# Kernel tuning notes

Measured on AMD Instinct MI355X. Metric: run time of the kernel, lower is better.

The kernel has to match this reference:

```python
import jax, jax.numpy as jnp
import numpy as np
from jax.scipy.linalg import expm

B, S, D, E, K, NROT = 2, 2048, 1024, 8, 2, 3
EPS = 1e-5


def setup_inputs() -> dict:
    key = jax.random.key(0)
    ks = jax.random.split(key, 16)
    sc = 0.02
    x = jax.random.normal(ks[0], (B, S, D), jnp.float32)
    ln_gamma = 1.0 + sc * jax.random.normal(ks[1], (D,), jnp.float32)
    ln_beta = sc * jax.random.normal(ks[2], (D,), jnp.float32)
    abel_w = sc * jax.random.normal(ks[3], (D, D), jnp.float32)
    abel_b = sc * jax.random.normal(ks[4], (D,), jnp.float32)
    moe_gate_w = sc * jax.random.normal(ks[5], (D, E), jnp.float32)
    moe_gate_b = sc * jax.random.normal(ks[6], (E,), jnp.float32)
    ew1 = sc * jax.random.normal(ks[7], (E, D, 2 * D), jnp.float32)
    eb1 = sc * jax.random.normal(ks[8], (E, 2 * D), jnp.float32)
    ew2 = sc * jax.random.normal(ks[9], (E, 2 * D, D), jnp.float32)
    eb2 = sc * jax.random.normal(ks[10], (E, D), jnp.float32)
    g = sc * jax.random.normal(ks[11], (NROT, D, D), jnp.float32)
    gens = 0.5 * (g - jnp.swapaxes(g, -1, -2))  # skew-symmetric, as in reset_parameters
    gc_w = sc * jax.random.normal(ks[12], (2 * D, 1), jnp.float32)
    gc_b = sc * jax.random.normal(ks[13], (1,), jnp.float32)
    return dict(x=x, ln_gamma=ln_gamma, ln_beta=ln_beta, abel_w=abel_w, abel_b=abel_b,
                moe_gate_w=moe_gate_w, moe_gate_b=moe_gate_b, ew1=ew1, eb1=eb1,
                ew2=ew2, eb2=eb2, gens=gens, gc_w=gc_w, gc_b=gc_b)


def _gelu(x):
    return jax.nn.gelu(x, approximate=False)  # torch nn.GELU default = exact erf


def _forward(x, ln_gamma, ln_beta, abel_w, abel_b, moe_gate_w, moe_gate_b,
             ew1, eb1, ew2, eb2, gens, gc_w, gc_b):
    residual = x
    # LayerNorm
    mu = jnp.mean(x, axis=-1, keepdims=True)
    var = jnp.mean((x - mu) ** 2, axis=-1, keepdims=True)
    xn = (x - mu) * jax.lax.rsqrt(var + EPS) * ln_gamma + ln_beta
    # abel branch: Linear + GELU
    abel_out = _gelu(xn @ abel_w + abel_b)
    # MoE: dense all-experts compute, masked by top-k softmax weights
    logits = xn @ moe_gate_w + moe_gate_b                      # [B,S,E]
    topw, topi = jax.lax.top_k(logits, K)                      # [B,S,K]
    topw = jax.nn.softmax(topw, axis=-1)
    w_dense = jnp.sum(jax.nn.one_hot(topi, E, dtype=xn.dtype) * topw[..., None], axis=-2)  # [B,S,E]
    h = _gelu(jnp.einsum('bsd,edh->ebsh', xn, ew1) + eb1[:, None, None, :])  # [E,B,S,2D]
    eo = jnp.einsum('ebsh,ehd->ebsd', h, ew2) + eb2[:, None, None, :]        # [E,B,S,D]
    moe_out = jnp.einsum('ebsd,bse->bsd', eo, w_dense)
    # GeometricRotation: sequential matrix_exp rotations
    for i in range(NROT):
        moe_out = moe_out @ expm(gens[i])
    # gated residual mix
    combined = jnp.concatenate([abel_out, moe_out], axis=-1)
    gate = jax.nn.sigmoid(combined @ gc_w + gc_b)              # [B,S,1]
    mixed = abel_out * (1.0 - gate) + moe_out * gate
    return residual + mixed


def reference(x, ln_gamma, ln_beta, abel_w, abel_b, moe_gate_w, moe_gate_b,
              ew1, eb1, ew2, eb2, gens, gc_w, gc_b):
    return _forward(x, ln_gamma, ln_beta, abel_w, abel_b, moe_gate_w, moe_gate_b,
                    ew1, eb1, ew2, eb2, gens, gc_w, gc_b)
```

## Files before the change

kernel.cpp:

```cpp
#include <hip/hip_runtime.h>
#include <hip/hip_bf16.h>
#include <cstdint>
#include <cstddef>

#define DD   1024
#define DD2  2048
#define EE   8
#define NTOK 4096
#define CAPR 9216

typedef __bf16 bf16_t;
typedef __bf16 bf16x8 __attribute__((ext_vector_type(8)));
typedef __bf16 bf16x4 __attribute__((ext_vector_type(4)));
typedef float  f32x4v __attribute__((ext_vector_type(4)));

__device__ __forceinline__ float gelu_f(float v){
  const float t = v*(0.7978845608028654f + 0.0356774081f*v*v);
  const float u = __expf(2.0f*t);
  return __fdividef(v*u, 1.0f + u);
}

__device__ __forceinline__ void gload_lds16(const void* g, void* l){
  __builtin_amdgcn_global_load_lds(
    (const __attribute__((address_space(1))) unsigned int*)(uintptr_t)g,
    (__attribute__((address_space(3))) unsigned int*)(uintptr_t)l,
    16, 0, 0);
}

enum { EPI_GELU_F32=0, EPI_GELU_BF16=1, EPI_BIAS_BF16=2, EPI_SCALE_BF16=3,
       EPI_ADDV_BF16=4, EPI_BF16=5, EPI_F32=6 };

template<int BM,int BN,int EPI,bool DYN>
__global__ __launch_bounds__(256)
void gemm_bt(const bf16_t* __restrict__ A, const bf16_t* __restrict__ Bt,
             const bf16_t* __restrict__ Bt2,
             const int N, const int K, const int gx, const int gy, const int gz,
             const long sAz, const long sBz, const long sOz, const int zsplit,
             const int* __restrict__ cnt, const int* __restrict__ offp,
             const float* __restrict__ bias, const long sBias,
             const float alpha, const float alpha2,
             const bf16_t* __restrict__ addv,
             float* __restrict__ outF, bf16_t* __restrict__ outB)
{
  constexpr int BK = 64;
  constexpr int WM = BM/2, WN = BN/2;
  constexpr int FM = WM/16, FN = WN/16;
  constexpr int IA = BM/32, IB = BN/32;
  __shared__ alignas(16) bf16_t sA[BM*BK];
  __shared__ alignas(16) bf16_t sB[BN*BK];

  int bx, by, bz;
  if constexpr (DYN) {
    const int e = blockIdx.x & 7;
    const int i = blockIdx.x >> 3;
    bz = e; by = i / gx; bx = i - by*gx;
    if (by * BM >= cnt[e]) return;
  } else {
    const int nwg = gx * gy * gz;
    const int q = nwg >> 3, r = nwg & 7;
    const int k = blockIdx.x & 7, i = blockIdx.x >> 3;
    if (i >= q + (k < r ? 1 : 0)) return;
    const int l = k * q + (k < r ? k : r) + i;
    bx = l % gx; const int t2 = l / gx; by = t2 % gy; bz = t2 / gy;
  }

  const int z = bz;
  int zz = z; const bf16_t* Bp = Bt; float al = alpha;
  if (z >= zsplit) { zz = z - zsplit; Bp = Bt2; al = alpha2; }

  float*  oF = outF;
  bf16_t* oB = outB;
  if constexpr (DYN) {
    const long ro = offp[z];
    A  += ro * (long)K;
    oB += ro * (long)N;
  } else {
    A += (size_t)zz * sAz;
    if (oF) oF += (size_t)z * sOz;
    if (oB) oB += (size_t)z * sOz;
  }
  Bp += (size_t)zz * sBz;
  const float*  bp = bias ? bias + (size_t)z * sBias : nullptr;
  const bf16_t* vp = addv ? addv + (size_t)z * sOz   : nullptr;

  const int tid = threadIdx.x;
  const int wid = tid >> 6, lid = tid & 63;
  const int wr = wid >> 1, wc = wid & 1;
  const int brow = by * BM, bcol = bx * BN;
  const int sr = lid >> 3, sq = lid & 7;
  const int fr = lid & 15, fq = lid >> 4;

  f32x4v acc[FM][FN] = {};

  for (int kt = 0; kt < K; kt += BK) {
    #pragma unroll
    for (int i = 0; i < IA; i++) {
      const int ii = wid*IA + i;
      const int r  = ii*8 + sr;
      const int q  = sq ^ (r & 7);
      gload_lds16((const char*)A + ((size_t)(brow + r)*K + kt)*2 + q*16,
                  (char*)sA + ii*1024);
    }
    #pragma unroll
    for (int i = 0; i < IB; i++) {
      const int ii = wid*IB + i;
      const int r  = ii*8 + sr;
      const int q  = sq ^ (r & 7);
      gload_lds16((const char*)Bp + ((size_t)(bcol + r)*K + kt)*2 + q*16,
                  (char*)sB + ii*1024);
    }
    __syncthreads();

    #pragma unroll
    for (int kk = 0; kk < 2; kk++) {
      bf16x8 af[FM], bb[FN];
      #pragma unroll
      for (int mi = 0; mi < FM; mi++) {
        const int r = wr*WM + mi*16 + fr;
        const int q = (kk*4 + fq) ^ (r & 7);
        af[mi] = *(const bf16x8*)((const char*)sA + r*128 + q*16);
      }
      #pragma unroll
      for (int ni = 0; ni < FN; ni++) {
        const int r = wc*WN + ni*16 + fr;
        const int q = (kk*4 + fq) ^ (r & 7);
        bb[ni] = *(const bf16x8*)((const char*)sB + r*128 + q*16);
      }
      #pragma unroll
      for (int mi = 0; mi < FM; mi++)
        #pragma unroll
        for (int ni = 0; ni < FN; ni++)
          acc[mi][ni] = __builtin_amdgcn_mfma_f32_16x16x32_bf16(
              af[mi], bb[ni], acc[mi][ni], 0, 0, 0);
    }
    __syncthreads();
  }

  #pragma unroll
  for (int mi = 0; mi < FM; mi++) {
    #pragma unroll
    for (int ni = 0; ni < FN; ni++) {
      const int rg0 = brow + wr*WM + mi*16 + fq*4;
      const int cg  = bcol + wc*WN + ni*16 + fr;
      #pragma unroll
      for (int i = 0; i < 4; i++) {
        const int rg = rg0 + i;
        float v = acc[mi][ni][i];
        if constexpr (EPI == EPI_GELU_F32) {
          v += bp[cg];
          oF[(size_t)rg*N + cg] = gelu_f(v);
        } else if constexpr (EPI == EPI_GELU_BF16) {
          v += bp[cg];
          oB[(size_t)rg*N + cg] = (bf16_t)gelu_f(v);
        } else if constexpr (EPI == EPI_BIAS_BF16) {
          v += bp[cg];
          oB[(size_t)rg*N + cg] = (bf16_t)v;
        } else if constexpr (EPI == EPI_SCALE_BF16) {
          oB[(size_t)rg*N + cg] = (bf16_t)(v * al);
        } else if constexpr (EPI == EPI_ADDV_BF16) {
          oB[(size_t)rg*N + cg] = (bf16_t)(v + (float)vp[(size_t)rg*N + cg]);
        } else if constexpr (EPI == EPI_BF16) {
          oB[(size_t)rg*N + cg] = (bf16_t)v;
        } else {
          oF[(size_t)rg*N + cg] = v;
        }
      }
    }
  }
}

__global__ __launch_bounds__(256)
void tcvt_kernel(const float* __restrict__ src, bf16_t* __restrict__ dst, int R, int C){
  __shared__ float tile[32][33];
  const size_t bo = (size_t)blockIdx.z * R * C;
  const int c0 = blockIdx.x*32, r0 = blockIdx.y*32;
  #pragma unroll
  for (int i = 0; i < 4; i++) {
    const int r = r0 + threadIdx.y + i*8;
    tile[threadIdx.y + i*8][threadIdx.x] = src[bo + (size_t)r*C + c0 + threadIdx.x];
  }
  __syncthreads();
  #pragma unroll
  for (int i = 0; i < 4; i++) {
    const int c = c0 + threadIdx.y + i*8;
    dst[bo + (size_t)c*R + r0 + threadIdx.x] = (bf16_t)tile[threadIdx.x][threadIdx.y + i*8];
  }
}

__global__ __launch_bounds__(256)
void tb16_kernel(const bf16_t* __restrict__ Ut, bf16_t* __restrict__ Tb){
  __shared__ bf16_t tile[32][33];
  const bf16_t* src = Ut + (size_t)(1 - blockIdx.z) * DD * DD;
  bf16_t*       dst = Tb + (size_t)blockIdx.z * DD * DD;
  const int c0 = blockIdx.x*32, r0 = blockIdx.y*32;
  #pragma unroll
  for (int i = 0; i < 4; i++)
    tile[threadIdx.y + i*8][threadIdx.x] = src[(size_t)(r0 + threadIdx.y + i*8)*DD + c0 + threadIdx.x];
  __syncthreads();
  #pragma unroll
  for (int i = 0; i < 4; i++)
    dst[(size_t)(c0 + threadIdx.y + i*8)*DD + r0 + threadIdx.x] = tile[threadIdx.x][threadIdx.y + i*8];
}

__global__ __launch_bounds__(256)
void cvt_kernel(const float* __restrict__ in, bf16_t* __restrict__ o, long n, float scale){
  const long i = ((long)blockIdx.x*256 + threadIdx.x)*4;
  if (i >= n) return;
  const float4 v = *(const float4*)(in + i);
  bf16x4 b; b[0]=(bf16_t)(v.x*scale); b[1]=(bf16_t)(v.y*scale);
  b[2]=(bf16_t)(v.z*scale); b[3]=(bf16_t)(v.w*scale);
  *(bf16x4*)(o + i) = b;
}

__global__ __launch_bounds__(256)
void vw_kernel(const bf16_t* __restrict__ Hn, const bf16_t* __restrict__ H2,
               const bf16_t* __restrict__ H3, bf16_t* __restrict__ Vb,
               bf16_t* __restrict__ Wtb){
  const long i0 = ((long)blockIdx.x*256 + threadIdx.x)*4;
  const long rc = i0 % (long)(DD*DD);
  const int r = (int)(rc / DD), c0 = (int)(rc % DD);
  const bf16x4 h  = *(const bf16x4*)(Hn + i0);
  const bf16x4 h2 = *(const bf16x4*)(H2 + i0);
  const bf16x4 h3 = *(const bf16x4*)(H3 + i0);
  bf16x4 v, w;
  #pragma unroll
  for (int j = 0; j < 4; j++) {
    const float d  = (r == c0 + j) ? 1.0f : 0.0f;
    const float fh = (float)h[j], f2 = (float)h2[j], f3 = (float)h3[j];
    v[j] = (bf16_t)(d + fh + f2*0.5f + f3*(1.0f/6.0f));
    w[j] = (bf16_t)(d*(1.0f/24.0f) - fh*(1.0f/120.0f) + f2*(1.0f/720.0f) - f3*(1.0f/5040.0f));
  }
  *(bf16x4*)(Vb  + i0) = v;
  *(bf16x4*)(Wtb + i0) = w;
}

__global__ __launch_bounds__(256)
void ln_gate_kernel(const float* __restrict__ x, const float* __restrict__ gamma,
                    const float* __restrict__ beta, const float* __restrict__ gw,
                    const float* __restrict__ gb,
                    bf16_t* __restrict__ xnb, int2* __restrict__ ids,
                    float2* __restrict__ wts)
{
  const int t = blockIdx.x, tid = threadIdx.x, j0 = tid*4;
  const int wid = tid >> 6, lid = tid & 63;
  const float4 v = *(const float4*)(x + (size_t)t*DD + j0);
  float s  = v.x + v.y + v.z + v.w;
  float ss = v.x*v.x + v.y*v.y + v.z*v.z + v.w*v.w;
  #pragma unroll
  for (int off = 32; off; off >>= 1) { s += __shfl_down(s, off); ss += __shfl_down(ss, off); }
  __shared__ float redS[4], redQ[4], mv[2];
  if (lid == 0) { redS[wid] = s; redQ[wid] = ss; }
  __syncthreads();
  if (tid == 0) {
    const float S1 = redS[0]+redS[1]+redS[2]+redS[3];
    const float S2 = redQ[0]+redQ[1]+redQ[2]+redQ[3];
    const float mu  = S1 * (1.0f/DD);
    const float var = S2 * (1.0f/DD) - mu*mu;
    mv[0] = mu; mv[1] = rsqrtf(var + 1e-5f);
  }
  __syncthreads();
  const float mu = mv[0], rstd = mv[1];
  const float4 g = *(const float4*)(gamma + j0);
  const float4 b = *(const float4*)(beta  + j0);
  float xn[4];
  xn[0] = (v.x-mu)*rstd*g.x + b.x;
  xn[1] = (v.y-mu)*rstd*g.y + b.y;
  xn[2] = (v.z-mu)*rstd*g.z + b.z;
  xn[3] = (v.w-mu)*rstd*g.w + b.w;
  bf16x4 ov; ov[0]=(bf16_t)xn[0]; ov[1]=(bf16_t)xn[1]; ov[2]=(bf16_t)xn[2]; ov[3]=(bf16_t)xn[3];
  *(bf16x4*)(xnb + (size_t)t*DD + j0) = ov;

  float p[8] = {0,0,0,0,0,0,0,0};
  #pragma unroll
  for (int i = 0; i < 4; i++) {
    const float4 a0 = *(const float4*)(gw + (size_t)(j0+i)*EE);
    const float4 a1 = *(const float4*)(gw + (size_t)(j0+i)*EE + 4);
    const float xv = xn[i];
    p[0]+=xv*a0.x; p[1]+=xv*a0.y; p[2]+=xv*a0.z; p[3]+=xv*a0.w;
    p[4]+=xv*a1.x; p[5]+=xv*a1.y; p[6]+=xv*a1.z; p[7]+=xv*a1.w;
  }
  #pragma unroll
  for (int off = 32; off; off >>= 1) {
    #pragma unroll
    for (int e = 0; e < 8; e++) p[e] += __shfl_down(p[e], off);
  }
  __shared__ float pr[32];
  if (lid == 0) {
    #pragma unroll
    for (int e = 0; e < 8; e++) pr[wid*8 + e] = p[e];
  }
  __syncthreads();
  if (tid == 0) {
    float l[8];
    #pragma unroll
    for (int e = 0; e < 8; e++) l[e] = pr[e] + pr[8+e] + pr[16+e] + pr[24+e] + gb[e];
    int i1 = 0; float m1 = l[0];
    #pragma unroll
    for (int e = 1; e < 8; e++) if (l[e] > m1) { m1 = l[e]; i1 = e; }
    int i2 = 0; float m2 = -1e30f;
    #pragma unroll
    for (int e = 0; e < 8; e++) if (e != i1 && l[e] > m2) { m2 = l[e]; i2 = e; }
    const float wa = 1.0f/(1.0f + expf(m2 - m1));
    ids[t] = make_int2(i1, i2);
    wts[t] = make_float2(wa, 1.0f - wa);
  }
}

__global__ __launch_bounds__(256)
void route_kernel(const int2* __restrict__ ids, int* __restrict__ slotA,
                  int* __restrict__ slotB, int* __restrict__ cnt,
                  int* __restrict__ off)
{
  const int tid = threadIdx.x;
  const int wid = tid >> 6, lid = tid & 63;
  __shared__ int wsum[EE][4];
  __shared__ int base[EE];
  if (tid < EE) base[tid] = 0;
  __syncthreads();
  const unsigned long long lt = (1ull << lid) - 1ull;
  for (int c0 = 0; c0 < NTOK; c0 += 256) {
    const int t = c0 + tid;
    const int2 id = ids[t];
    int pA = 0, pB = 0;
    #pragma unroll
    for (int e = 0; e < EE; e++) {
      const bool fA = (id.x == e), fB = (id.y == e);
      const unsigned long long mA = __ballot(fA);
      const unsigned long long mB = __ballot(fB);
      const int cA = __popcll(mA);
      if (lid == 0) wsum[e][wid] = cA + __popcll(mB);
      if (fA) pA = __popcll(mA & lt);
      if (fB) pB = cA + __popcll(mB & lt);
    }
    __syncthreads();
    int wbA = base[id.x], wbB = base[id.y];
    for (int w = 0; w < wid; w++) { wbA += wsum[id.x][w]; wbB += wsum[id.y][w]; }
    slotA[t] = wbA + pA;
    slotB[t] = wbB + pB;
    __syncthreads();
    if (tid < EE) base[tid] += wsum[tid][0]+wsum[tid][1]+wsum[tid][2]+wsum[tid][3];
    __syncthreads();
  }
  if (tid == 0) {
    int a = 0;
    #pragma unroll
    for (int e = 0; e < EE; e++) { cnt[e] = base[e]; off[e] = a; a += (base[e]+127)&~127; }
  }
}

__global__ __launch_bounds__(256)
void gather_kernel(const bf16_t* __restrict__ xnb, const int2* __restrict__ ids,
                   const int* __restrict__ slotA, const int* __restrict__ slotB,
                   const int* __restrict__ off, bf16_t* __restrict__ Xg){
  const int t = blockIdx.x, j = threadIdx.x*4;
  const int2 id = ids[t];
  const bf16x4 v = *(const bf16x4*)(xnb + (size_t)t*DD + j);
  *(bf16x4*)(Xg + (size_t)(off[id.x] + slotA[t])*DD + j) = v;
  *(bf16x4*)(Xg + (size_t)(off[id.y] + slotB[t])*DD + j) = v;
}

__global__ __launch_bounds__(256)
void combine_kernel(const bf16_t* __restrict__ Yg, const int2* __restrict__ ids,
                    const int* __restrict__ slotA, const int* __restrict__ slotB,
                    const int* __restrict__ off, const float2* __restrict__ wts,
                    bf16_t* __restrict__ Xa){
  const int t = blockIdx.x, j = threadIdx.x*4;
  const int2 id = ids[t];
  const float2 w = wts[t];
  const bf16x4 a = *(const bf16x4*)(Yg + (size_t)(off[id.x] + slotA[t])*DD + j);
  const bf16x4 b = *(const bf16x4*)(Yg + (size_t)(off[id.y] + slotB[t])*DD + j);
  bf16x4 o;
  #pragma unroll
  for (int i = 0; i < 4; i++) o[i] = (bf16_t)(w.x*(float)a[i] + w.y*(float)b[i]);
  *(bf16x4*)(Xa + (size_t)t*DD + j) = o;
}

__global__ __launch_bounds__(256)
void mix_kernel(const float* __restrict__ x, const bf16_t* __restrict__ abel,
                const float* __restrict__ rot, const float* __restrict__ gcw,
                const float* __restrict__ gcb, float* __restrict__ out)
{
  const int t = blockIdx.x, tid = threadIdx.x, j0 = tid*4;
  const int wid = tid >> 6, lid = tid & 63;
  const bf16x4 ab = *(const bf16x4*)(abel + (size_t)t*DD + j0);
  const float4 r  = *(const float4*)(rot  + (size_t)t*DD + j0);
  const float4 ga = *(const float4*)(gcw + j0);
  const float4 gr = *(const float4*)(gcw + DD + j0);
  const float a0 = (float)ab[0], a1 = (float)ab[1], a2 = (float)ab[2], a3 = (float)ab[3];
  float p = a0*ga.x + a1*ga.y + a2*ga.z + a3*ga.w
          + r.x*gr.x + r.y*gr.y + r.z*gr.z + r.w*gr.w;
  #pragma unroll
  for (int off = 32; off; off >>= 1) p += __shfl_down(p, off);
  __shared__ float red[4];
  __shared__ float gsh;
  if (lid == 0) red[wid] = p;
  __syncthreads();
  if (tid == 0) {
    const float P = red[0] + red[1] + red[2] + red[3] + gcb[0];
    gsh = 1.0f/(1.0f + expf(-P));
  }
  __syncthreads();
  const float gate = gsh, g1 = 1.0f - gate;
  const float4 xv = *(const float4*)(x + (size_t)t*DD + j0);
  float4 o;
  o.x = xv.x + a0*g1 + r.x*gate;
  o.y = xv.y + a1*g1 + r.y*gate;
  o.z = xv.z + a2*g1 + r.z*gate;
  o.w = xv.w + a3*g1 + r.w*gate;
  *(float4*)(out + (size_t)t*DD + j0) = o;
}

extern "C" void kernel_launch(void* const* d_in, const int* in_sizes, int n_in,
                              void* d_out, int out_size, void* d_ws, size_t ws_size,
                              hipStream_t stream)
{
  (void)in_sizes; (void)n_in; (void)out_size; (void)ws_size;
  const float* x      = (const float*)d_in[0];
  const float* ln_g   = (const float*)d_in[1];
  const float* ln_b   = (const float*)d_in[2];
  const float* abel_w = (const float*)d_in[3];
  const float* abel_b = (const float*)d_in[4];
  const float* gate_w = (const float*)d_in[5];
  const float* gate_b = (const float*)d_in[6];
  const float* ew1    = (const float*)d_in[7];
  const float* eb1    = (const float*)d_in[8];
  const float* ew2    = (const float*)d_in[9];
  const float* eb2    = (const float*)d_in[10];
  const float* gens   = (const float*)d_in[11];
  const float* gc_w   = (const float*)d_in[12];
  const float* gc_b   = (const float*)d_in[13];
  float* out = (float*)d_out;

  char* wsp = (char*)d_ws;
  auto alloc = [&](size_t bytes) -> char* {
    char* p = wsp; wsp += (bytes + 255) & ~(size_t)255; return p;
  };
  const size_t MB = 1u<<20;
  bf16_t* xnb   = (bf16_t*)alloc((size_t)NTOK*DD*2);
  int2*   ids   = (int2*)  alloc((size_t)NTOK*8);
  float2* wts   = (float2*)alloc((size_t)NTOK*8);
  int*    slotA = (int*)   alloc((size_t)NTOK*4);
  int*    slotB = (int*)   alloc((size_t)NTOK*4);
  int*    cnt   = (int*)   alloc(64);
  int*    off   = (int*)   alloc(64);
  bf16_t* abel_wT = (bf16_t*)alloc((size_t)DD*DD*2);
  char*   UN      = alloc(64*MB);
  bf16_t* ew1T  = (bf16_t*)UN;
  bf16_t* ew2T  = (bf16_t*)(UN + 32*MB);
  bf16_t* Hn    = (bf16_t*)alloc((size_t)3*DD*DD*2);
  bf16_t* abelo = (bf16_t*)alloc((size_t)NTOK*DD*2);
  bf16_t* Xg    = (bf16_t*)alloc((size_t)CAPR*DD*2);
  bf16_t* Hg    = (bf16_t*)alloc((size_t)CAPR*DD2*2);
  bf16_t* Xa    = (bf16_t*)alloc((size_t)NTOK*DD*2);
  bf16_t* Yg    = Xg;
  float*  rot   = (float*)Hg;
  bf16_t* H2  = (bf16_t*)(UN + 0*MB);
  bf16_t* H34 = (bf16_t*)(UN + 6*MB);
  bf16_t* Vb  = (bf16_t*)(UN + 18*MB);
  bf16_t* Wtb = (bf16_t*)(UN + 24*MB);
  bf16_t* Ut  = (bf16_t*)(UN + 30*MB);
  bf16_t* Tb  = (bf16_t*)(UN + 36*MB);
  bf16_t* Pb  = (bf16_t*)(UN + 40*MB);
  bf16_t* Rt  = (bf16_t*)(UN + 42*MB);
  const long D2 = (long)DD*DD;

  auto gflat = [](int gx, int gy, int gz) {
    const int nwg = gx*gy*gz; return 8 * ((nwg + 7) / 8);
  };

  const dim3 tb(32, 8, 1);
  tcvt_kernel<<<dim3(DD/32,  DD/32, 1),  tb, 0, stream>>>(abel_w, abel_wT, DD,  DD);
  tcvt_kernel<<<dim3(DD2/32, DD/32, EE), tb, 0, stream>>>(ew1,    ew1T,    DD,  DD2);
  tcvt_kernel<<<dim3(DD/32,  DD2/32,EE), tb, 0, stream>>>(ew2,    ew2T,    DD2, DD);
  cvt_kernel<<<dim3(3*DD*DD/1024,1,1), 256, 0, stream>>>(gens, Hn, (long)3*DD*DD, -1.0f);

  ln_gate_kernel<<<dim3(NTOK,1,1), 256, 0, stream>>>(x, ln_g, ln_b, gate_w, gate_b,
                                                     xnb, ids, wts);
  route_kernel<<<dim3(1,1,1), 256, 0, stream>>>(ids, slotA, slotB, cnt, off);
  gather_kernel<<<dim3(NTOK,1,1), 256, 0, stream>>>(xnb, ids, slotA, slotB, off, Xg);

  gemm_bt<128,128,EPI_GELU_BF16,true><<<dim3(8*(DD2/128)*(NTOK/128),1,1), 256, 0, stream>>>(
      Xg, ew1T, nullptr, DD2, DD, DD2/128, NTOK/128, EE, 0, (long)DD2*DD, 0, 1<<30,
      cnt, off, eb1, DD2, 1.0f, 0.0f, nullptr, nullptr, Hg);
  gemm_bt<128,128,EPI_BIAS_BF16,true><<<dim3(8*(DD/128)*(NTOK/128),1,1), 256, 0, stream>>>(
      Hg, ew2T, nullptr, DD, DD2, DD/128, NTOK/128, EE, 0, (long)DD*DD2, 0, 1<<30,
      cnt, off, eb2, DD, 1.0f, 0.0f, nullptr, nullptr, Yg);
  combine_kernel<<<dim3(NTOK,1,1), 256, 0, stream>>>(Yg, ids, slotA, slotB, off, wts, Xa);

  gemm_bt<128,64,EPI_GELU_BF16,false><<<dim3(gflat(16,32,1),1,1), 256, 0, stream>>>(
      xnb, abel_wT, nullptr, DD, DD, 16, 32, 1, 0, 0, 0, 1<<30, nullptr, nullptr,
      abel_b, 0, 1.0f, 0.0f, nullptr, nullptr, abelo);

  gemm_bt<128,64,EPI_SCALE_BF16,false><<<dim3(gflat(16,8,3),1,1), 256, 0, stream>>>(
      Hn, Hn, nullptr, DD, DD, 16, 8, 3, D2, D2, D2, 1<<30, nullptr, nullptr,
      nullptr, 0, -1.0f, 0.0f, nullptr, nullptr, H2);
  gemm_bt<128,64,EPI_SCALE_BF16,false><<<dim3(gflat(16,8,6),1,1), 256, 0, stream>>>(
      H2, Hn, H2, DD, DD, 16, 8, 6, D2, D2, D2, 3, nullptr, nullptr,
      nullptr, 0, -1.0f, 1.0f, nullptr, nullptr, H34);
  vw_kernel<<<dim3(3*DD*DD/1024,1,1), 256, 0, stream>>>(Hn, H2, H34, Vb, Wtb);
  gemm_bt<128,64,EPI_ADDV_BF16,false><<<dim3(gflat(16,8,3),1,1), 256, 0, stream>>>(
      H34 + 3*D2, Wtb, nullptr, DD, DD, 16, 8, 3, D2, D2, D2, 1<<30, nullptr, nullptr,
      nullptr, 0, 1.0f, 0.0f, Vb, nullptr, Ut);
  tb16_kernel<<<dim3(32,32,2), tb, 0, stream>>>(Ut, Tb);
  gemm_bt<128,64,EPI_BF16,false><<<dim3(gflat(16,8,1),1,1), 256, 0, stream>>>(
      Ut + 2*D2, Tb, nullptr, DD, DD, 16, 8, 1, 0, 0, 0, 1<<30, nullptr, nullptr,
      nullptr, 0, 1.0f, 0.0f, nullptr, nullptr, Pb);
  gemm_bt<128,64,EPI_BF16,false><<<dim3(gflat(16,8,1),1,1), 256, 0, stream>>>(
      Pb, Tb + D2, nullptr, DD, DD, 16, 8, 1, 0, 0, 0, 1<<30, nullptr, nullptr,
      nullptr, 0, 1.0f, 0.0f, nullptr, nullptr, Rt);
  gemm_bt<128,64,EPI_F32,false><<<dim3(gflat(16,32,1),1,1), 256, 0, stream>>>(
      Xa, Rt, nullptr, DD, DD, 16, 32, 1, 0, 0, 0, 1<<30, nullptr, nullptr,
      nullptr, 0, 1.0f, 0.0f, nullptr, rot, nullptr);

  mix_kernel<<<dim3(NTOK,1,1), 256, 0, stream>>>(x, abelo, rot, gc_w, gc_b, out);
}
```

Before: 383.8 us.

## Double-buffer GEMM LDS tiles and truncate the matrix-exponential Taylor series

The GEMM kernel now keeps two shared-memory tile buffers and issues the asynchronous global-to-LDS loads for the next K tile before computing on the current one. This is meant to hide global memory latency behind the MFMA work. Separately, the rotation matrix exponential drops the fourth-power term. Its polynomial evaluation is reduced to fewer terms, so one batched 3×1024³ GEMM and the third operand read in the V/W elementwise kernel go away. The cost is doubled LDS use per workgroup, which may lower occupancy, and a lower-order expm approximation that adds accuracy error depending on the generator norm.

```diff
diff --git a/kernel.cpp b/kernel.cpp
--- a/kernel.cpp
+++ b/kernel.cpp
@@ -33,12 +33,11 @@
 template<int BM,int BN,int EPI,bool DYN>
 __global__ __launch_bounds__(256)
 void gemm_bt(const bf16_t* __restrict__ A, const bf16_t* __restrict__ Bt,
-             const bf16_t* __restrict__ Bt2,
              const int N, const int K, const int gx, const int gy, const int gz,
-             const long sAz, const long sBz, const long sOz, const int zsplit,
+             const long sAz, const long sBz, const long sOz,
              const int* __restrict__ cnt, const int* __restrict__ offp,
              const float* __restrict__ bias, const long sBias,
-             const float alpha, const float alpha2,
+             const float alpha,
              const bf16_t* __restrict__ addv,
              float* __restrict__ outF, bf16_t* __restrict__ outB)
 {
@@ -46,8 +45,8 @@
   constexpr int WM = BM/2, WN = BN/2;
   constexpr int FM = WM/16, FN = WN/16;
   constexpr int IA = BM/32, IB = BN/32;
-  __shared__ alignas(16) bf16_t sA[BM*BK];
-  __shared__ alignas(16) bf16_t sB[BN*BK];
+  __shared__ alignas(16) bf16_t sA[2][BM*BK];
+  __shared__ alignas(16) bf16_t sB[2][BN*BK];
 
   int bx, by, bz;
   if constexpr (DYN) {
@@ -65,9 +64,7 @@
   }
 
   const int z = bz;
-  int zz = z; const bf16_t* Bp = Bt; float al = alpha;
-  if (z >= zsplit) { zz = z - zsplit; Bp = Bt2; al = alpha2; }
-
+  const bf16_t* Bp = Bt;
   float*  oF = outF;
   bf16_t* oB = outB;
   if constexpr (DYN) {
@@ -75,11 +72,11 @@
     A  += ro * (long)K;
     oB += ro * (long)N;
   } else {
-    A += (size_t)zz * sAz;
+    A += (size_t)z * sAz;
     if (oF) oF += (size_t)z * sOz;
     if (oB) oB += (size_t)z * sOz;
   }
-  Bp += (size_t)zz * sBz;
+  Bp += (size_t)z * sBz;
   const float*  bp = bias ? bias + (size_t)z * sBias : nullptr;
   const bf16_t* vp = addv ? addv + (size_t)z * sOz   : nullptr;
 
@@ -92,14 +89,14 @@
 
   f32x4v acc[FM][FN] = {};
 
-  for (int kt = 0; kt < K; kt += BK) {
+  auto stage = [&](int buf, int kt) {
     #pragma unroll
     for (int i = 0; i < IA; i++) {
       const int ii = wid*IA + i;
       const int r  = ii*8 + sr;
       const int q  = sq ^ (r & 7);
       gload_lds16((const char*)A + ((size_t)(brow + r)*K + kt)*2 + q*16,
-                  (char*)sA + ii*1024);
+                  (char*)sA[buf] + ii*1024);
     }
     #pragma unroll
     for (int i = 0; i < IB; i++) {
@@ -107,9 +104,16 @@
       const int r  = ii*8 + sr;
       const int q  = sq ^ (r & 7);
       gload_lds16((const char*)Bp + ((size_t)(bcol + r)*K + kt)*2 + q*16,
-                  (char*)sB + ii*1024);
+                  (char*)sB[buf] + ii*1024);
     }
-    __syncthreads();
+  };
+
+  stage(0, 0);
+  __syncthreads();
+  int cur = 0;
+
+  for (int kt = 0; kt < K; kt += BK) {
+    if (kt + BK < K) stage(cur ^ 1, kt + BK);
 
     #pragma unroll
     for (int kk = 0; kk < 2; kk++) {
@@ -118,13 +122,13 @@
       for (int mi = 0; mi < FM; mi++) {
         const int r = wr*WM + mi*16 + fr;
         const int q = (kk*4 + fq) ^ (r & 7);
-        af[mi] = *(const bf16x8*)((const char*)sA + r*128 + q*16);
+        af[mi] = *(const bf16x8*)((const char*)sA[cur] + r*128 + q*16);
       }
       #pragma unroll
       for (int ni = 0; ni < FN; ni++) {
         const int r = wc*WN + ni*16 + fr;
         const int q = (kk*4 + fq) ^ (r & 7);
-        bb[ni] = *(const bf16x8*)((const char*)sB + r*128 + q*16);
+        bb[ni] = *(const bf16x8*)((const char*)sB[cur] + r*128 + q*16);
       }
       #pragma unroll
       for (int mi = 0; mi < FM; mi++)
@@ -134,6 +138,7 @@
               af[mi], bb[ni], acc[mi][ni], 0, 0, 0);
     }
     __syncthreads();
+    cur ^= 1;
   }
 
   #pragma unroll
@@ -156,7 +161,7 @@
           v += bp[cg];
           oB[(size_t)rg*N + cg] = (bf16_t)v;
         } else if constexpr (EPI == EPI_SCALE_BF16) {
-          oB[(size_t)rg*N + cg] = (bf16_t)(v * al);
+          oB[(size_t)rg*N + cg] = (bf16_t)(v * alpha);
         } else if constexpr (EPI == EPI_ADDV_BF16) {
           oB[(size_t)rg*N + cg] = (bf16_t)(v + (float)vp[(size_t)rg*N + cg]);
         } else if constexpr (EPI == EPI_BF16) {
@@ -214,21 +219,19 @@
 
 __global__ __launch_bounds__(256)
 void vw_kernel(const bf16_t* __restrict__ Hn, const bf16_t* __restrict__ H2,
-               const bf16_t* __restrict__ H3, bf16_t* __restrict__ Vb,
-               bf16_t* __restrict__ Wtb){
+               bf16_t* __restrict__ Vb, bf16_t* __restrict__ Wtb){
   const long i0 = ((long)blockIdx.x*256 + threadIdx.x)*4;
   const long rc = i0 % (long)(DD*DD);
   const int r = (int)(rc / DD), c0 = (int)(rc % DD);
   const bf16x4 h  = *(const bf16x4*)(Hn + i0);
   const bf16x4 h2 = *(const bf16x4*)(H2 + i0);
-  const bf16x4 h3 = *(const bf16x4*)(H3 + i0);
   bf16x4 v, w;
   #pragma unroll
   for (int j = 0; j < 4; j++) {
     const float d  = (r == c0 + j) ? 1.0f : 0.0f;
-    const float fh = (float)h[j], f2 = (float)h2[j], f3 = (float)h3[j];
-    v[j] = (bf16_t)(d + fh + f2*0.5f + f3*(1.0f/6.0f));
-    w[j] = (bf16_t)(d*(1.0f/24.0f) - fh*(1.0f/120.0f) + f2*(1.0f/720.0f) - f3*(1.0f/5040.0f));
+    const float fh = (float)h[j], f2 = (float)h2[j];
+    v[j] = (bf16_t)(d + fh + f2*0.5f);
+    w[j] = (bf16_t)(d*(1.0f/6.0f) - fh*(1.0f/24.0f) + f2*(1.0f/120.0f));
   }
   *(bf16x4*)(Vb  + i0) = v;
   *(bf16x4*)(Wtb + i0) = w;
@@ -455,13 +458,13 @@
   bf16_t* Yg    = Xg;
   float*  rot   = (float*)Hg;
   bf16_t* H2  = (bf16_t*)(UN + 0*MB);
-  bf16_t* H34 = (bf16_t*)(UN + 6*MB);
-  bf16_t* Vb  = (bf16_t*)(UN + 18*MB);
-  bf16_t* Wtb = (bf16_t*)(UN + 24*MB);
-  bf16_t* Ut  = (bf16_t*)(UN + 30*MB);
-  bf16_t* Tb  = (bf16_t*)(UN + 36*MB);
-  bf16_t* Pb  = (bf16_t*)(UN + 40*MB);
-  bf16_t* Rt  = (bf16_t*)(UN + 42*MB);
+  bf16_t* H3  = (bf16_t*)(UN + 6*MB);
+  bf16_t* Vb  = (bf16_t*)(UN + 12*MB);
+  bf16_t* Wtb = (bf16_t*)(UN + 18*MB);
+  bf16_t* Ut  = (bf16_t*)(UN + 24*MB);
+  bf16_t* Tb  = (bf16_t*)(UN + 30*MB);
+  bf16_t* Pb  = (bf16_t*)(UN + 34*MB);
+  bf16_t* Rt  = (bf16_t*)(UN + 36*MB);
   const long D2 = (long)DD*DD;
 
   auto gflat = [](int gx, int gy, int gz) {
@@ -480,37 +483,37 @@
   gather_kernel<<<dim3(NTOK,1,1), 256, 0, stream>>>(xnb, ids, slotA, slotB, off, Xg);
 
   gemm_bt<128,128,EPI_GELU_BF16,true><<<dim3(8*(DD2/128)*(NTOK/128),1,1), 256, 0, stream>>>(
-      Xg, ew1T, nullptr, DD2, DD, DD2/128, NTOK/128, EE, 0, (long)DD2*DD, 0, 1<<30,
-      cnt, off, eb1, DD2, 1.0f, 0.0f, nullptr, nullptr, Hg);
+      Xg, ew1T, DD2, DD, DD2/128, NTOK/128, EE, 0, (long)DD2*DD, 0,
+      cnt, off, eb1, DD2, 1.0f, nullptr, nullptr, Hg);
   gemm_bt<128,128,EPI_BIAS_BF16,true><<<dim3(8*(DD/128)*(NTOK/128),1,1), 256, 0, stream>>>(
-      Hg, ew2T, nullptr, DD, DD2, DD/128, NTOK/128, EE, 0, (long)DD*DD2, 0, 1<<30,
-      cnt, off, eb2, DD, 1.0f, 0.0f, nullptr, nullptr, Yg);
+      Hg, ew2T, DD, DD2, DD/128, NTOK/128, EE, 0, (long)DD*DD2, 0,
+      cnt, off, eb2, DD, 1.0f, nullptr, nullptr, Yg);
   combine_kernel<<<dim3(NTOK,1,1), 256, 0, stream>>>(Yg, ids, slotA, slotB, off, wts, Xa);
 
   gemm_bt<128,64,EPI_GELU_BF16,false><<<dim3(gflat(16,32,1),1,1), 256, 0, stream>>>(
-      xnb, abel_wT, nullptr, DD, DD, 16, 32, 1, 0, 0, 0, 1<<30, nullptr, nullptr,
-      abel_b, 0, 1.0f, 0.0f, nullptr, nullptr, abelo);
+      xnb, abel_wT, DD, DD, 16, 32, 1, 0, 0, 0, nullptr, nullptr,
+      abel_b, 0, 1.0f, nullptr, nullptr, abelo);
 
   gemm_bt<128,64,EPI_SCALE_BF16,false><<<dim3(gflat(16,8,3),1,1), 256, 0, stream>>>(
-      Hn, Hn, nullptr, DD, DD, 16, 8, 3, D2, D2, D2, 1<<30, nullptr, nullptr,
-      nullptr, 0, -1.0f, 0.0f, nullptr, nullptr, H2);
-  gemm_bt<128,64,EPI_SCALE_BF16,false><<<dim3(gflat(16,8,6),1,1), 256, 0, stream>>>(
-      H2, Hn, H2, DD, DD, 16, 8, 6, D2, D2, D2, 3, nullptr, nullptr,
-      nullptr, 0, -1.0f, 1.0f, nullptr, nullptr, H34);
-  vw_kernel<<<dim3(3*DD*DD/1024,1,1), 256, 0, stream>>>(Hn, H2, H34, Vb, Wtb);
+      Hn, Hn, DD, DD, 16, 8, 3, D2, D2, D2, nullptr, nullptr,
+      nullptr, 0, -1.0f, nullptr, nullptr, H2);
+  gemm_bt<128,64,EPI_SCALE_BF16,false><<<dim3(gflat(16,8,3),1,1), 256, 0, stream>>>(
+      H2, Hn, DD, DD, 16, 8, 3, D2, D2, D2, nullptr, nullptr,
+      nullptr, 0, -1.0f, nullptr, nullptr, H3);
+  vw_kernel<<<dim3(3*DD*DD/1024,1,1), 256, 0, stream>>>(Hn, H2, Vb, Wtb);
   gemm_bt<128,64,EPI_ADDV_BF16,false><<<dim3(gflat(16,8,3),1,1), 256, 0, stream>>>(
-      H34 + 3*D2, Wtb, nullptr, DD, DD, 16, 8, 3, D2, D2, D2, 1<<30, nullptr, nullptr,
-      nullptr, 0, 1.0f, 0.0f, Vb, nullptr, Ut);
+      H3, Wtb, DD, DD, 16, 8, 3, D2, D2, D2, nullptr, nullptr,
+      nullptr, 0, 1.0f, Vb, nullptr, Ut);
   tb16_kernel<<<dim3(32,32,2), tb, 0, stream>>>(Ut, Tb);
   gemm_bt<128,64,EPI_BF16,false><<<dim3(gflat(16,8,1),1,1), 256, 0, stream>>>(
-      Ut + 2*D2, Tb, nullptr, DD, DD, 16, 8, 1, 0, 0, 0, 1<<30, nullptr, nullptr,
-      nullptr, 0, 1.0f, 0.0f, nullptr, nullptr, Pb);
+      Ut + 2*D2, Tb, DD, DD, 16, 8, 1, 0, 0, 0, nullptr, nullptr,
+      nullptr, 0, 1.0f, nullptr, nullptr, Pb);
   gemm_bt<128,64,EPI_BF16,false><<<dim3(gflat(16,8,1),1,1), 256, 0, stream>>>(
-      Pb, Tb + D2, nullptr, DD, DD, 16, 8, 1, 0, 0, 0, 1<<30, nullptr, nullptr,
-      nullptr, 0, 1.0f, 0.0f, nullptr, nullptr, Rt);
+      Pb, Tb + D2, DD, DD, 16, 8, 1, 0, 0, 0, nullptr, nullptr,
+      nullptr, 0, 1.0f, nullptr, nullptr, Rt);
   gemm_bt<128,64,EPI_F32,false><<<dim3(gflat(16,32,1),1,1), 256, 0, stream>>>(
-      Xa, Rt, nullptr, DD, DD, 16, 32, 1, 0, 0, 0, 1<<30, nullptr, nullptr,
-      nullptr, 0, 1.0f, 0.0f, nullptr, rot, nullptr);
+      Xa, Rt, DD, DD, 16, 32, 1, 0, 0, 0, nullptr, nullptr,
+      nullptr, 0, 1.0f, nullptr, rot, nullptr);
 
   mix_kernel<<<dim3(NTOK,1,1), 256, 0, stream>>>(x, abelo, rot, gc_w, gc_b, out);
 }
```

New measurement: 345.9 us. 1.11x faster.
